# Performance work log

Hardware: AMD Instinct MI355X
Metric: run time of the kernel (lower is better)

The kernel has to match this reference:

```python
import jax, jax.numpy as jnp
import numpy as np

N_INPUT, N_HIDDEN, N_OUTPUT = 64, 512, 24

def setup_inputs() -> dict:
    key = jax.random.key(0)
    ks = jax.random.split(key, 7)
    s_ih = 1.0 / np.sqrt(N_HIDDEN)
    x = jax.random.normal(ks[0], (256, 512, N_INPUT), dtype=jnp.float32)
    W_ih = jax.random.uniform(ks[1], (N_HIDDEN, N_INPUT), minval=-s_ih, maxval=s_ih, dtype=jnp.float32)
    W_hh = jax.random.uniform(ks[2], (N_HIDDEN, N_HIDDEN), minval=-s_ih, maxval=s_ih, dtype=jnp.float32)
    b_ih = jax.random.uniform(ks[3], (N_HIDDEN,), minval=-s_ih, maxval=s_ih, dtype=jnp.float32)
    b_hh = jax.random.uniform(ks[4], (N_HIDDEN,), minval=-s_ih, maxval=s_ih, dtype=jnp.float32)
    W_ho = jax.random.uniform(ks[5], (N_OUTPUT, N_HIDDEN), minval=-s_ih, maxval=s_ih, dtype=jnp.float32)
    b_ho = jax.random.uniform(ks[6], (N_OUTPUT,), minval=-s_ih, maxval=s_ih, dtype=jnp.float32)
    return {"x": x, "W_ih": W_ih, "W_hh": W_hh, "b_ih": b_ih, "b_hh": b_hh, "W_ho": W_ho, "b_ho": b_ho}

def reference(x, W_ih, W_hh, b_ih, b_hh, W_ho, b_ho):
    B = x.shape[0]
    # Precompute input projections for all timesteps in one big GEMM: [B,T,H]
    xp = jnp.einsum('bti,hi->bth', x, W_ih) + b_ih + b_hh
    h0 = jnp.zeros((B, W_hh.shape[0]), dtype=x.dtype)

    def step(h, xp_t):
        h = jnp.tanh(xp_t + h @ W_hh.T)
        out = jnp.tanh(h @ W_ho.T + b_ho)
        return h, out

    _, outs = jax.lax.scan(step, h0, jnp.swapaxes(xp, 0, 1))  # outs: [T,B,O]
    return jnp.swapaxes(outs, 0, 1)  # [B,T,O]
```

## Files before the change

### kernel.cpp

```cpp
#include <hip/hip_runtime.h>
#include <cstdint>
#include <cstddef>


#define TSTEPS 512
#define HDIM   512
#define NIN    64
#define NOUT   24
#define BB     16
#define HPAD   520
#define XPAD   72
#define NREG   49
#define NLDS   (64 - NREG)
#define NREG_B 50
#define NLDS_B (64 - NREG_B)

typedef _Float16 h16;
typedef __attribute__((ext_vector_type(8))) _Float16 h16x8;
typedef __attribute__((ext_vector_type(4))) _Float16 h16x4;
typedef __attribute__((ext_vector_type(2))) _Float16 h16x2;
typedef __attribute__((ext_vector_type(4))) float    f32x4;
typedef __attribute__((ext_vector_type(2))) float    f32x2;

__device__ __forceinline__ float fast_tanh(float z) {
  float e = __builtin_amdgcn_exp2f(z * 2.8853900817779268f);
  return 1.0f - 2.0f * __builtin_amdgcn_rcpf(e + 1.0f);
}

__device__ __forceinline__ h16x8 cvt8(const float* __restrict__ p) {
  f32x4 f0 = *(const f32x4*)p;
  f32x4 f1 = *(const f32x4*)(p + 4);
  h16x8 a;
  #pragma unroll
  for (int j = 0; j < 4; ++j) { a[j] = (h16)f0[j]; a[4 + j] = (h16)f1[j]; }
  return a;
}

__global__ __launch_bounds__(512)
void xp_gemm(const float* __restrict__ x, const float* __restrict__ Wih,
             const float* __restrict__ bih, const float* __restrict__ bhh,
             h16* __restrict__ xp)
{
  const int tid  = threadIdx.x;
  const int wave = tid >> 6;
  const int lane = tid & 63;
  const int lr   = lane & 15;
  const int lk   = lane >> 4;
  const int blk  = blockIdx.x & 15;
  const int tc   = blockIdx.x >> 4;
  const int c0   = wave * 64;

  h16x8 A[4][2];
  #pragma unroll
  for (int m = 0; m < 4; ++m)
    #pragma unroll
    for (int s = 0; s < 2; ++s)
      A[m][s] = cvt8(Wih + (size_t)(c0 + 16 * m + lr) * NIN + 32 * s + 8 * lk);

  f32x4 bias[4];
  #pragma unroll
  for (int m = 0; m < 4; ++m) {
    const int c = c0 + 16 * m + 4 * lk;
    f32x4 bi = *(const f32x4*)&bih[c];
    f32x4 bh = *(const f32x4*)&bhh[c];
    bias[m] = bi + bh;
  }

  const float* xrow = x + (size_t)(16 * blk + lr) * (TSTEPS * NIN);

  for (int j = 0; j < 32; ++j) {
    const int t = tc * 32 + j;
    f32x4 acc[4];
    #pragma unroll
    for (int m = 0; m < 4; ++m) acc[m] = bias[m];
    #pragma unroll
    for (int s = 0; s < 2; ++s) {
      h16x8 bx = cvt8(xrow + (size_t)t * NIN + 32 * s + 8 * lk);
      #pragma unroll
      for (int m = 0; m < 4; ++m)
        acc[m] = __builtin_amdgcn_mfma_f32_16x16x32_f16(A[m][s], bx, acc[m], 0, 0, 0);
    }
    h16x8 c0v, c1v;
    #pragma unroll
    for (int i = 0; i < 4; ++i) {
      c0v[i]     = (h16)acc[0][i];
      c0v[4 + i] = (h16)acc[1][i];
      c1v[i]     = (h16)acc[2][i];
      c1v[4 + i] = (h16)acc[3][i];
    }
    h16* p = xp + ((((size_t)t * 16 + blk) * 8 + wave) * 64 + lane) * 16;
    *(h16x8*)p       = c0v;
    *(h16x8*)(p + 8) = c1v;
  }
}

__global__ __launch_bounds__(512, 2)
void rnn_core(const float* __restrict__ Whh, const h16* __restrict__ xp,
              h16* __restrict__ hall)
{
  __shared__ h16 hbuf[2][BB * HPAD];
  __shared__ h16 aslice[NLDS * 8 * 512];

  const int tid  = threadIdx.x;
  const int wave = tid >> 6;
  const int lane = tid & 63;
  const int lr   = lane & 15;
  const int lk   = lane >> 4;
  const int blk  = blockIdx.x;
  const int b0   = blk * BB;
  const int wc0  = wave * 64;

  h16x8 areg[NREG];
  #pragma unroll
  for (int s = 0; s < 16; ++s) {
    #pragma unroll
    for (int m = 0; m < 4; ++m) {
      h16x8 a = cvt8(Whh + (size_t)(wc0 + 16 * m + lr) * HDIM + 32 * s + 8 * lk);
      const int id = s * 4 + m;
      if (id < NREG) areg[id] = a;
      else *(h16x8*)&aslice[(size_t)((id - NREG) * 8 + wave) * 512 + lane * 8] = a;
    }
  }

  for (int idx = tid; idx < BB * HPAD; idx += 512) hbuf[0][idx] = (h16)0.f;
  __syncthreads();

  h16x8 xr0, xr1;
  {
    const h16* p = xp + (((size_t)blk * 8 + wave) * 64 + lane) * 16;
    xr0 = *(const h16x8*)p;
    xr1 = *(const h16x8*)(p + 8);
  }

  for (int t = 0; t < TSTEPS; ++t) {
    const h16* hb = hbuf[t & 1];
    h16*       hn = hbuf[(t + 1) & 1];

    f32x4 acc[4];
    #pragma unroll
    for (int i = 0; i < 4; ++i) {
      acc[0][i] = (float)xr0[i];
      acc[1][i] = (float)xr0[4 + i];
      acc[2][i] = (float)xr1[i];
      acc[3][i] = (float)xr1[4 + i];
    }

    {
      const int tn = (t + 1 < TSTEPS) ? (t + 1) : t;
      const h16* p = xp + ((((size_t)tn * 16 + blk) * 8 + wave) * 64 + lane) * 16;
      xr0 = *(const h16x8*)p;
      xr1 = *(const h16x8*)(p + 8);
    }

    #pragma unroll
    for (int s = 0; s < 16; ++s) {
      h16x8 bh = *(const h16x8*)&hb[lr * HPAD + 32 * s + 8 * lk];
      #pragma unroll
      for (int m = 0; m < 4; ++m) {
        const int id = s * 4 + m;
        h16x8 a = (id < NREG)
            ? areg[id]
            : *(const h16x8*)&aslice[(size_t)((id - NREG) * 8 + wave) * 512 + lane * 8];
        acc[m] = __builtin_amdgcn_mfma_f32_16x16x32_f16(a, bh, acc[m], 0, 0, 0);
      }
    }

    h16* hrow = hall + ((size_t)t * 256 + b0 + lr) * HDIM + wc0 + lk * 4;
    #pragma unroll
    for (int m = 0; m < 4; ++m) {
      h16x4 hv;
      #pragma unroll
      for (int i = 0; i < 4; ++i) hv[i] = (h16)fast_tanh(acc[m][i]);
      *(h16x4*)&hn[lr * HPAD + wc0 + 16 * m + 4 * lk] = hv;
      *(h16x4*)(hrow + 16 * m) = hv;
    }

    __syncthreads();
  }
}

__global__ __launch_bounds__(512)
void out_all(const h16* __restrict__ hall, const float* __restrict__ Who,
             const float* __restrict__ bho, float* __restrict__ out)
{
  __shared__ h16 wholds[NOUT * HPAD];

  const int tid  = threadIdx.x;
  const int wave = tid >> 6;
  const int lane = tid & 63;
  const int lr   = lane & 15;
  const int lk   = lane >> 4;

  for (int idx = tid; idx < NOUT * HDIM; idx += 512) {
    int r = idx >> 9, k = idx & 511;
    wholds[r * HPAD + k] = (h16)Who[idx];
  }

  f32x4 o0, o1;
  { o0 = *(const f32x4*)&bho[lk * 4]; }
  { int ob = 16 + lk * 4;
    if (ob < NOUT) o1 = *(const f32x4*)&bho[ob];
    else { o1[0] = 0.f; o1[1] = 0.f; o1[2] = 0.f; o1[3] = 0.f; } }
  __syncthreads();

  const int rt = blockIdx.x * 8 + wave;
  const int t  = rt >> 4;
  const int b  = (rt & 15) * 16 + lr;
  const int row1 = (16 + lr < NOUT) ? (16 + lr) : (8 + lr);

  const h16* hrow = hall + ((size_t)t * 256 + b) * HDIM + lk * 8;

  #pragma unroll
  for (int s = 0; s < 16; ++s) {
    h16x8 bh = *(const h16x8*)(hrow + 32 * s);
    h16x8 a0 = *(const h16x8*)&wholds[lr * HPAD + s * 32 + lk * 8];
    h16x8 a1 = *(const h16x8*)&wholds[row1 * HPAD + s * 32 + lk * 8];
    o0 = __builtin_amdgcn_mfma_f32_16x16x32_f16(a0, bh, o0, 0, 0, 0);
    o1 = __builtin_amdgcn_mfma_f32_16x16x32_f16(a1, bh, o1, 0, 0, 0);
  }

  float* op = out + ((size_t)b * TSTEPS + t) * NOUT;
  f32x4 v0;
  #pragma unroll
  for (int i = 0; i < 4; ++i) v0[i] = fast_tanh(o0[i]);
  *(f32x4*)(op + lk * 4) = v0;
  if (lk < 2) {
    f32x4 v1;
    #pragma unroll
    for (int i = 0; i < 4; ++i) v1[i] = fast_tanh(o1[i]);
    *(f32x4*)(op + 16 + lk * 4) = v1;
  }
}

__device__ __forceinline__ void out_proj(
    int t, const h16* __restrict__ hb, const h16* __restrict__ who,
    f32x4 bho0, f32x4 bho1, float* __restrict__ out, int b0, int lr, int lk)
{
  f32x4 o0 = bho0, o1 = bho1;
  const int row1 = (16 + lr < NOUT) ? (16 + lr) : (8 + lr);
  #pragma unroll
  for (int s = 0; s < 16; ++s) {
    h16x8 bh = *(const h16x8*)&hb[lr * HPAD + s * 32 + lk * 8];
    h16x8 a0 = *(const h16x8*)&who[lr * HPAD + s * 32 + lk * 8];
    h16x8 a1 = *(const h16x8*)&who[row1 * HPAD + s * 32 + lk * 8];
    o0 = __builtin_amdgcn_mfma_f32_16x16x32_f16(a0, bh, o0, 0, 0, 0);
    o1 = __builtin_amdgcn_mfma_f32_16x16x32_f16(a1, bh, o1, 0, 0, 0);
  }
  float* op = out + ((size_t)(b0 + lr) * TSTEPS + t) * NOUT;
  f32x4 v0;
  #pragma unroll
  for (int i = 0; i < 4; ++i) v0[i] = fast_tanh(o0[i]);
  *(f32x4*)(op + lk * 4) = v0;
  if (lk < 2) {
    f32x4 v1;
    #pragma unroll
    for (int i = 0; i < 4; ++i) v1[i] = fast_tanh(o1[i]);
    *(f32x4*)(op + 16 + lk * 4) = v1;
  }
}

__global__ __launch_bounds__(512, 2)
void rnn_fast2(const float* __restrict__ Whh, const float* __restrict__ Who,
               const float* __restrict__ bho, const h16* __restrict__ xp,
               float* __restrict__ out)
{
  __shared__ h16 hls[BB * HPAD];
  __shared__ h16 wholds[NOUT * HPAD];
  __shared__ h16 aslice[NLDS_B * 8 * 512];

  const int tid  = threadIdx.x;
  const int wave = tid >> 6;
  const int lane = tid & 63;
  const int lr   = lane & 15;
  const int lk   = lane >> 4;
  const int blk  = blockIdx.x;
  const int b0   = blk * BB;
  const int wc0  = wave * 64;

  h16x8 areg[NREG_B];
  #pragma unroll
  for (int s = 0; s < 16; ++s) {
    #pragma unroll
    for (int m = 0; m < 4; ++m) {
      h16x8 a = cvt8(Whh + (size_t)(wc0 + 16 * m + lr) * HDIM + 32 * s + 8 * lk);
      const int id = s * 4 + m;
      if (id < NREG_B) areg[id] = a;
      else *(h16x8*)&aslice[(size_t)((id - NREG_B) * 8 + wave) * 512 + lane * 8] = a;
    }
  }

  f32x4 bho0, bho1;
  { bho0 = *(const f32x4*)&bho[lk * 4]; }
  { int ob = 16 + lk * 4;
    if (ob < NOUT) bho1 = *(const f32x4*)&bho[ob];
    else { bho1[0] = 0.f; bho1[1] = 0.f; bho1[2] = 0.f; bho1[3] = 0.f; } }

  for (int idx = tid; idx < NOUT * HDIM; idx += 512) {
    int r = idx >> 9, k = idx & 511;
    wholds[r * HPAD + k] = (h16)Who[idx];
  }
  for (int idx = tid; idx < BB * HPAD; idx += 512) hls[idx] = (h16)0.f;
  __syncthreads();

  h16x8 xr0, xr1;
  {
    const h16* p = xp + (((size_t)blk * 8 + wave) * 64 + lane) * 16;
    xr0 = *(const h16x8*)p;
    xr1 = *(const h16x8*)(p + 8);
  }

  for (int t = 0; t < TSTEPS; ++t) {
    if (t > 0 && wave == ((t - 1) & 7))
      out_proj(t - 1, hls, wholds, bho0, bho1, out, b0, lr, lk);

    f32x4 acc[4];
    #pragma unroll
    for (int i = 0; i < 4; ++i) {
      acc[0][i] = (float)xr0[i];
      acc[1][i] = (float)xr0[4 + i];
      acc[2][i] = (float)xr1[i];
      acc[3][i] = (float)xr1[4 + i];
    }
    {
      const int tn = (t + 1 < TSTEPS) ? (t + 1) : t;
      const h16* p = xp + ((((size_t)tn * 16 + blk) * 8 + wave) * 64 + lane) * 16;
      xr0 = *(const h16x8*)p;
      xr1 = *(const h16x8*)(p + 8);
    }
    #pragma unroll
    for (int s = 0; s < 16; ++s) {
      h16x8 bh = *(const h16x8*)&hls[lr * HPAD + 32 * s + 8 * lk];
      #pragma unroll
      for (int m = 0; m < 4; ++m) {
        const int id = s * 4 + m;
        h16x8 a = (id < NREG_B)
            ? areg[id]
            : *(const h16x8*)&aslice[(size_t)((id - NREG_B) * 8 + wave) * 512 + lane * 8];
        acc[m] = __builtin_amdgcn_mfma_f32_16x16x32_f16(a, bh, acc[m], 0, 0, 0);
      }
    }
    __syncthreads();
    #pragma unroll
    for (int m = 0; m < 4; ++m) {
      h16x4 hv;
      #pragma unroll
      for (int i = 0; i < 4; ++i) hv[i] = (h16)fast_tanh(acc[m][i]);
      *(h16x4*)&hls[lr * HPAD + wc0 + 16 * m + 4 * lk] = hv;
    }
    __syncthreads();
  }

  if (wave == ((TSTEPS - 1) & 7))
    out_proj(TSTEPS - 1, hls, wholds, bho0, bho1, out, b0, lr, lk);
}

__global__ __launch_bounds__(512, 2)
void rnn_fused(const float* __restrict__ x,
               const float* __restrict__ Wih,
               const float* __restrict__ Whh,
               const float* __restrict__ bih,
               const float* __restrict__ bhh,
               const float* __restrict__ Who,
               const float* __restrict__ bho,
               float* __restrict__ out)
{
  __shared__ h16 hbuf[2][BB * HPAD];
  __shared__ h16 xbuf[2][BB * XPAD];
  __shared__ h16 wholds[NOUT * HPAD];

  const int tid  = threadIdx.x;
  const int wave = tid >> 6;
  const int lane = tid & 63;
  const int lr   = lane & 15;
  const int lk   = lane >> 4;
  const int b0   = blockIdx.x * BB;
  const int wc0  = wave * 64;

  h16x8 a_rec[4][16];
  #pragma unroll
  for (int m = 0; m < 4; ++m) {
    const int row = wc0 + m * 16 + lr;
    #pragma unroll
    for (int s = 0; s < 16; ++s)
      a_rec[m][s] = cvt8(Whh + (size_t)row * HDIM + s * 32 + lk * 8);
  }
  h16x8 a_ih[4][2];
  #pragma unroll
  for (int m = 0; m < 4; ++m) {
    const int row = wc0 + m * 16 + lr;
    #pragma unroll
    for (int s = 0; s < 2; ++s)
      a_ih[m][s] = cvt8(Wih + (size_t)row * NIN + s * 32 + lk * 8);
  }
  f32x4 biasv[4];
  #pragma unroll
  for (int m = 0; m < 4; ++m) {
    const int c = wc0 + m * 16 + lk * 4;
    f32x4 bi = *(const f32x4*)&bih[c];
    f32x4 bh2 = *(const f32x4*)&bhh[c];
    biasv[m] = bi + bh2;
  }
  f32x4 bho0, bho1;
  { bho0 = *(const f32x4*)&bho[lk * 4]; }
  { int ob = 16 + lk * 4;
    if (ob < NOUT) bho1 = *(const f32x4*)&bho[ob];
    else { bho1[0] = 0.f; bho1[1] = 0.f; bho1[2] = 0.f; bho1[3] = 0.f; } }

  for (int idx = tid; idx < NOUT * HDIM; idx += 512) {
    int r = idx >> 9, k = idx & 511;
    wholds[r * HPAD + k] = (h16)Who[idx];
  }
  for (int idx = tid; idx < BB * HPAD; idx += 512) hbuf[0][idx] = (h16)0.f;
  {
    int r = tid >> 5, c2 = (tid & 31) * 2;
    f32x2 v = *(const f32x2*)(x + ((size_t)(b0 + r) * TSTEPS + 0) * NIN + c2);
    h16x2 pk = { (h16)v.x, (h16)v.y };
    *(h16x2*)&xbuf[0][r * XPAD + c2] = pk;
  }
  __syncthreads();

  for (int t = 0; t < TSTEPS; ++t) {
    const h16* hb = hbuf[t & 1];
    h16*       hn = hbuf[(t + 1) & 1];
    const h16* xb = xbuf[t & 1];
    h16*       xn = xbuf[(t + 1) & 1];

    if (t > 0 && wave == ((t - 1) & 7))
      out_proj(t - 1, hb, wholds, bho0, bho1, out, b0, lr, lk);

    const int tl = (t + 1 < TSTEPS) ? (t + 1) : (TSTEPS - 1);
    const int xr = tid >> 5, xc = (tid & 31) * 2;
    f32x2 xv = *(const f32x2*)(x + ((size_t)(b0 + xr) * TSTEPS + tl) * NIN + xc);

    f32x4 acc[4];
    #pragma unroll
    for (int m = 0; m < 4; ++m) acc[m] = biasv[m];
    #pragma unroll
    for (int s = 0; s < 2; ++s) {
      h16x8 bx = *(const h16x8*)&xb[lr * XPAD + s * 32 + lk * 8];
      #pragma unroll
      for (int m = 0; m < 4; ++m)
        acc[m] = __builtin_amdgcn_mfma_f32_16x16x32_f16(a_ih[m][s], bx, acc[m], 0, 0, 0);
    }
    #pragma unroll
    for (int s = 0; s < 16; ++s) {
      h16x8 bh = *(const h16x8*)&hb[lr * HPAD + s * 32 + lk * 8];
      #pragma unroll
      for (int m = 0; m < 4; ++m)
        acc[m] = __builtin_amdgcn_mfma_f32_16x16x32_f16(a_rec[m][s], bh, acc[m], 0, 0, 0);
    }
    #pragma unroll
    for (int m = 0; m < 4; ++m) {
      h16x4 hv;
      #pragma unroll
      for (int i = 0; i < 4; ++i) hv[i] = (h16)fast_tanh(acc[m][i]);
      *(h16x4*)&hn[lr * HPAD + wc0 + m * 16 + lk * 4] = hv;
    }
    {
      h16x2 pk = { (h16)xv.x, (h16)xv.y };
      *(h16x2*)&xn[xr * XPAD + xc] = pk;
    }
    __syncthreads();
  }

  if (wave == ((TSTEPS - 1) & 7))
    out_proj(TSTEPS - 1, hbuf[TSTEPS & 1], wholds, bho0, bho1, out, b0, lr, lk);
}

extern "C" void kernel_launch(void* const* d_in, const int* in_sizes, int n_in,
                              void* d_out, int out_size, void* d_ws, size_t ws_size,
                              hipStream_t stream) {
  (void)in_sizes; (void)n_in; (void)out_size;
  const float* x   = (const float*)d_in[0];
  const float* Wih = (const float*)d_in[1];
  const float* Whh = (const float*)d_in[2];
  const float* bih = (const float*)d_in[3];
  const float* bhh = (const float*)d_in[4];
  const float* Who = (const float*)d_in[5];
  const float* bho = (const float*)d_in[6];
  float* out = (float*)d_out;

  const size_t XP_BYTES   = (size_t)TSTEPS * 256 * HDIM * sizeof(h16);
  const size_t HALL_BYTES = (size_t)TSTEPS * 256 * HDIM * sizeof(h16);

  if (ws_size >= XP_BYTES + HALL_BYTES) {
    h16* xp   = (h16*)d_ws;
    h16* hall = (h16*)((char*)d_ws + XP_BYTES);
    xp_gemm<<<dim3(256), dim3(512), 0, stream>>>(x, Wih, bih, bhh, xp);
    rnn_core<<<dim3(256 / BB), dim3(512), 0, stream>>>(Whh, xp, hall);
    out_all<<<dim3(1024), dim3(512), 0, stream>>>(hall, Who, bho, out);
  } else if (ws_size >= XP_BYTES) {
    h16* xp = (h16*)d_ws;
    xp_gemm<<<dim3(256), dim3(512), 0, stream>>>(x, Wih, bih, bhh, xp);
    rnn_fast2<<<dim3(256 / BB), dim3(512), 0, stream>>>(Whh, Who, bho, xp, out);
  } else {
    rnn_fused<<<dim3(256 / BB), dim3(512), 0, stream>>>(x, Wih, Whh, bih, bhh, Who, bho, out);
  }
}
```

Measured before the change: 1.090 ms.

## Split recurrent GEMM K-dimension across block pairs with global-memory partial-sum exchange

Adds rnn_core2, which splits each batch group's recurrent matmul over two workgroups, each holding half of the K dimension of W_hh entirely in registers and so dropping the LDS-resident weight slice. Each step, the non-finishing waves write fp32 partial sums to a global exchange buffer and signal an atomic counter; the finishing waves spin-wait, add the partner's partials, apply tanh and write h. This doubles the number of CUs working on the recurrence (32 blocks instead of 16) at the cost of a cross-CU handshake through L2 every timestep. The counter is zeroed inside xp_gemm, and the rnn_fast2 fallback path is removed.

```diff
diff --git a/kernel.cpp b/kernel.cpp
--- a/kernel.cpp
+++ b/kernel.cpp
@@ -10,10 +10,10 @@
 #define BB     16
 #define HPAD   520
 #define XPAD   72
+#define KHALF  256
+#define HPAD2  264
 #define NREG   49
 #define NLDS   (64 - NREG)
-#define NREG_B 50
-#define NLDS_B (64 - NREG_B)
 
 typedef _Float16 h16;
 typedef __attribute__((ext_vector_type(8))) _Float16 h16x8;
@@ -39,7 +39,7 @@
 __global__ __launch_bounds__(512)
 void xp_gemm(const float* __restrict__ x, const float* __restrict__ Wih,
              const float* __restrict__ bih, const float* __restrict__ bhh,
-             h16* __restrict__ xp)
+             h16* __restrict__ xp, unsigned* __restrict__ cnt)
 {
   const int tid  = threadIdx.x;
   const int wave = tid >> 6;
@@ -50,6 +50,8 @@
   const int tc   = blockIdx.x >> 4;
   const int c0   = wave * 64;
 
+  if (cnt && blockIdx.x == 0 && tid < 64) cnt[tid] = 0u;
+
   h16x8 A[4][2];
   #pragma unroll
   for (int m = 0; m < 4; ++m)
@@ -91,6 +93,155 @@
     h16* p = xp + ((((size_t)t * 16 + blk) * 8 + wave) * 64 + lane) * 16;
     *(h16x8*)p       = c0v;
     *(h16x8*)(p + 8) = c1v;
+  }
+}
+
+__global__ __launch_bounds__(512, 2)
+void rnn_core2(const float* __restrict__ Whh, const h16* __restrict__ xp,
+               h16* __restrict__ hall, float* __restrict__ ex,
+               unsigned* __restrict__ cnt)
+{
+  __shared__ h16 hl[2][16 * HPAD2];
+
+  const int tid  = threadIdx.x;
+  const int wave = tid >> 6;
+  const int lane = tid & 63;
+  const int lr   = lane & 15;
+  const int lk   = lane >> 4;
+  const int kb   = blockIdx.x >> 4;
+  const int g    = blockIdx.x & 15;
+  const int wq   = wave & 3;
+  const bool fin = ((wave >> 2) == kb);
+  const int b0   = g * 16;
+
+  h16x8 areg[8][4];
+  #pragma unroll
+  for (int s = 0; s < 8; ++s)
+    #pragma unroll
+    for (int m = 0; m < 4; ++m)
+      areg[s][m] = cvt8(Whh + (size_t)(64 * wave + 16 * m + lr) * HDIM
+                        + KHALF * kb + 32 * s + 8 * lk);
+
+  for (int idx = tid; idx < 16 * HPAD2; idx += 512) hl[0][idx] = (h16)0.f;
+  __syncthreads();
+
+  h16x8 xr0, xr1;
+  if (fin) {
+    const h16* p = xp + (((size_t)g * 8 + wave) * 64 + lane) * 16;
+    xr0 = *(const h16x8*)p;
+    xr1 = *(const h16x8*)(p + 8);
+  }
+
+  unsigned* mycnt   = &cnt[g * 2 + kb];
+  unsigned* partcnt = &cnt[g * 2 + (1 - kb)];
+
+  for (int t = 0; t < TSTEPS; ++t) {
+    f32x4 acc[4];
+    if (fin) {
+      #pragma unroll
+      for (int i = 0; i < 4; ++i) {
+        acc[0][i] = (float)xr0[i];
+        acc[1][i] = (float)xr0[4 + i];
+        acc[2][i] = (float)xr1[i];
+        acc[3][i] = (float)xr1[4 + i];
+      }
+      const int tn = (t + 1 < TSTEPS) ? (t + 1) : t;
+      const h16* p = xp + ((((size_t)tn * 16 + g) * 8 + wave) * 64 + lane) * 16;
+      xr0 = *(const h16x8*)p;
+      xr1 = *(const h16x8*)(p + 8);
+    } else {
+      #pragma unroll
+      for (int m = 0; m < 4; ++m) { acc[m][0]=0.f; acc[m][1]=0.f; acc[m][2]=0.f; acc[m][3]=0.f; }
+    }
+
+    const h16* hb = hl[t & 1];
+    #pragma unroll
+    for (int s = 0; s < 8; ++s) {
+      h16x8 bh = *(const h16x8*)&hb[lr * HPAD2 + 32 * s + 8 * lk];
+      #pragma unroll
+      for (int m = 0; m < 4; ++m)
+        acc[m] = __builtin_amdgcn_mfma_f32_16x16x32_f16(areg[s][m], bh, acc[m], 0, 0, 0);
+    }
+
+    if (!fin) {
+      float* exw = ex + ((size_t)((g * 2 + kb) * 2 + (t & 1)) << 12);
+      #pragma unroll
+      for (int m = 0; m < 4; ++m)
+        *(f32x4*)&exw[((wq * 16 + m * 4 + lk) << 6) + lr * 4] = acc[m];
+      if (lane == 0)
+        __hip_atomic_fetch_add(mycnt, 1u, __ATOMIC_RELEASE, __HIP_MEMORY_SCOPE_AGENT);
+    } else {
+      const unsigned tgt = 4u * (unsigned)(t + 1);
+      while (__hip_atomic_load(partcnt, __ATOMIC_ACQUIRE, __HIP_MEMORY_SCOPE_AGENT) < tgt)
+        __builtin_amdgcn_s_sleep(1);
+      const float* exr = ex + ((size_t)((g * 2 + (1 - kb)) * 2 + (t & 1)) << 12);
+      h16* hn   = hl[(t + 1) & 1];
+      h16* hrow = hall + ((size_t)t * 256 + b0 + lr) * HDIM + KHALF * kb + 64 * wq + 4 * lk;
+      #pragma unroll
+      for (int m = 0; m < 4; ++m) {
+        f32x4 pp = *(const f32x4*)&exr[((wq * 16 + m * 4 + lk) << 6) + lr * 4];
+        h16x4 hv;
+        #pragma unroll
+        for (int i = 0; i < 4; ++i) hv[i] = (h16)fast_tanh(acc[m][i] + pp[i]);
+        *(h16x4*)&hn[lr * HPAD2 + 64 * wq + 16 * m + 4 * lk] = hv;
+        *(h16x4*)(hrow + 16 * m) = hv;
+      }
+    }
+
+    __syncthreads();
+  }
+}
+
+__global__ __launch_bounds__(512)
+void out_all(const h16* __restrict__ hall, const float* __restrict__ Who,
+             const float* __restrict__ bho, float* __restrict__ out)
+{
+  __shared__ h16 wholds[NOUT * HPAD];
+
+  const int tid  = threadIdx.x;
+  const int wave = tid >> 6;
+  const int lane = tid & 63;
+  const int lr   = lane & 15;
+  const int lk   = lane >> 4;
+
+  for (int idx = tid; idx < NOUT * HDIM; idx += 512) {
+    int r = idx >> 9, k = idx & 511;
+    wholds[r * HPAD + k] = (h16)Who[idx];
+  }
+
+  f32x4 o0, o1;
+  { o0 = *(const f32x4*)&bho[lk * 4]; }
+  { int ob = 16 + lk * 4;
+    if (ob < NOUT) o1 = *(const f32x4*)&bho[ob];
+    else { o1[0] = 0.f; o1[1] = 0.f; o1[2] = 0.f; o1[3] = 0.f; } }
+  __syncthreads();
+
+  const int rt = blockIdx.x * 8 + wave;
+  const int t  = rt >> 4;
+  const int b  = (rt & 15) * 16 + lr;
+  const int row1 = (16 + lr < NOUT) ? (16 + lr) : (8 + lr);
+
+  const h16* hrow = hall + ((size_t)t * 256 + b) * HDIM + lk * 8;
+
+  #pragma unroll
+  for (int s = 0; s < 16; ++s) {
+    h16x8 bh = *(const h16x8*)(hrow + 32 * s);
+    h16x8 a0 = *(const h16x8*)&wholds[lr * HPAD + s * 32 + lk * 8];
+    h16x8 a1 = *(const h16x8*)&wholds[row1 * HPAD + s * 32 + lk * 8];
+    o0 = __builtin_amdgcn_mfma_f32_16x16x32_f16(a0, bh, o0, 0, 0, 0);
+    o1 = __builtin_amdgcn_mfma_f32_16x16x32_f16(a1, bh, o1, 0, 0, 0);
+  }
+
+  float* op = out + ((size_t)b * TSTEPS + t) * NOUT;
+  f32x4 v0;
+  #pragma unroll
+  for (int i = 0; i < 4; ++i) v0[i] = fast_tanh(o0[i]);
+  *(f32x4*)(op + lk * 4) = v0;
+  if (lk < 2) {
+    f32x4 v1;
+    #pragma unroll
+    for (int i = 0; i < 4; ++i) v1[i] = fast_tanh(o1[i]);
+    *(f32x4*)(op + 16 + lk * 4) = v1;
   }
 }
 
@@ -144,7 +295,6 @@
       acc[2][i] = (float)xr1[i];
       acc[3][i] = (float)xr1[4 + i];
     }
-
     {
       const int tn = (t + 1 < TSTEPS) ? (t + 1) : t;
       const h16* p = xp + ((((size_t)tn * 16 + blk) * 8 + wave) * 64 + lane) * 16;
@@ -179,59 +329,6 @@
   }
 }
 
-__global__ __launch_bounds__(512)
-void out_all(const h16* __restrict__ hall, const float* __restrict__ Who,
-             const float* __restrict__ bho, float* __restrict__ out)
-{
-  __shared__ h16 wholds[NOUT * HPAD];
-
-  const int tid  = threadIdx.x;
-  const int wave = tid >> 6;
-  const int lane = tid & 63;
-  const int lr   = lane & 15;
-  const int lk   = lane >> 4;
-
-  for (int idx = tid; idx < NOUT * HDIM; idx += 512) {
-    int r = idx >> 9, k = idx & 511;
-    wholds[r * HPAD + k] = (h16)Who[idx];
-  }
-
-  f32x4 o0, o1;
-  { o0 = *(const f32x4*)&bho[lk * 4]; }
-  { int ob = 16 + lk * 4;
-    if (ob < NOUT) o1 = *(const f32x4*)&bho[ob];
-    else { o1[0] = 0.f; o1[1] = 0.f; o1[2] = 0.f; o1[3] = 0.f; } }
-  __syncthreads();
-
-  const int rt = blockIdx.x * 8 + wave;
-  const int t  = rt >> 4;
-  const int b  = (rt & 15) * 16 + lr;
-  const int row1 = (16 + lr < NOUT) ? (16 + lr) : (8 + lr);
-
-  const h16* hrow = hall + ((size_t)t * 256 + b) * HDIM + lk * 8;
-
-  #pragma unroll
-  for (int s = 0; s < 16; ++s) {
-    h16x8 bh = *(const h16x8*)(hrow + 32 * s);
-    h16x8 a0 = *(const h16x8*)&wholds[lr * HPAD + s * 32 + lk * 8];
-    h16x8 a1 = *(const h16x8*)&wholds[row1 * HPAD + s * 32 + lk * 8];
-    o0 = __builtin_amdgcn_mfma_f32_16x16x32_f16(a0, bh, o0, 0, 0, 0);
-    o1 = __builtin_amdgcn_mfma_f32_16x16x32_f16(a1, bh, o1, 0, 0, 0);
-  }
-
-  float* op = out + ((size_t)b * TSTEPS + t) * NOUT;
-  f32x4 v0;
-  #pragma unroll
-  for (int i = 0; i < 4; ++i) v0[i] = fast_tanh(o0[i]);
-  *(f32x4*)(op + lk * 4) = v0;
-  if (lk < 2) {
-    f32x4 v1;
-    #pragma unroll
-    for (int i = 0; i < 4; ++i) v1[i] = fast_tanh(o1[i]);
-    *(f32x4*)(op + 16 + lk * 4) = v1;
-  }
-}
-
 __device__ __forceinline__ void out_proj(
     int t, const h16* __restrict__ hb, const h16* __restrict__ who,
     f32x4 bho0, f32x4 bho1, float* __restrict__ out, int b0, int lr, int lk)
@@ -257,101 +354,6 @@
     for (int i = 0; i < 4; ++i) v1[i] = fast_tanh(o1[i]);
     *(f32x4*)(op + 16 + lk * 4) = v1;
   }
-}
-
-__global__ __launch_bounds__(512, 2)
-void rnn_fast2(const float* __restrict__ Whh, const float* __restrict__ Who,
-               const float* __restrict__ bho, const h16* __restrict__ xp,
-               float* __restrict__ out)
-{
-  __shared__ h16 hls[BB * HPAD];
-  __shared__ h16 wholds[NOUT * HPAD];
-  __shared__ h16 aslice[NLDS_B * 8 * 512];
-
-  const int tid  = threadIdx.x;
-  const int wave = tid >> 6;
-  const int lane = tid & 63;
-  const int lr   = lane & 15;
-  const int lk   = lane >> 4;
-  const int blk  = blockIdx.x;
-  const int b0   = blk * BB;
-  const int wc0  = wave * 64;
-
-  h16x8 areg[NREG_B];
-  #pragma unroll
-  for (int s = 0; s < 16; ++s) {
-    #pragma unroll
-    for (int m = 0; m < 4; ++m) {
-      h16x8 a = cvt8(Whh + (size_t)(wc0 + 16 * m + lr) * HDIM + 32 * s + 8 * lk);
-      const int id = s * 4 + m;
-      if (id < NREG_B) areg[id] = a;
-      else *(h16x8*)&aslice[(size_t)((id - NREG_B) * 8 + wave) * 512 + lane * 8] = a;
-    }
-  }
-
-  f32x4 bho0, bho1;
-  { bho0 = *(const f32x4*)&bho[lk * 4]; }
-  { int ob = 16 + lk * 4;
-    if (ob < NOUT) bho1 = *(const f32x4*)&bho[ob];
-    else { bho1[0] = 0.f; bho1[1] = 0.f; bho1[2] = 0.f; bho1[3] = 0.f; } }
-
-  for (int idx = tid; idx < NOUT * HDIM; idx += 512) {
-    int r = idx >> 9, k = idx & 511;
-    wholds[r * HPAD + k] = (h16)Who[idx];
-  }
-  for (int idx = tid; idx < BB * HPAD; idx += 512) hls[idx] = (h16)0.f;
-  __syncthreads();
-
-  h16x8 xr0, xr1;
-  {
-    const h16* p = xp + (((size_t)blk * 8 + wave) * 64 + lane) * 16;
-    xr0 = *(const h16x8*)p;
-    xr1 = *(const h16x8*)(p + 8);
-  }
-
-  for (int t = 0; t < TSTEPS; ++t) {
-    if (t > 0 && wave == ((t - 1) & 7))
-      out_proj(t - 1, hls, wholds, bho0, bho1, out, b0, lr, lk);
-
-    f32x4 acc[4];
-    #pragma unroll
-    for (int i = 0; i < 4; ++i) {
-      acc[0][i] = (float)xr0[i];
-      acc[1][i] = (float)xr0[4 + i];
-      acc[2][i] = (float)xr1[i];
-      acc[3][i] = (float)xr1[4 + i];
-    }
-    {
-      const int tn = (t + 1 < TSTEPS) ? (t + 1) : t;
-      const h16* p = xp + ((((size_t)tn * 16 + blk) * 8 + wave) * 64 + lane) * 16;
-      xr0 = *(const h16x8*)p;
-      xr1 = *(const h16x8*)(p + 8);
-    }
-    #pragma unroll
-    for (int s = 0; s < 16; ++s) {
-      h16x8 bh = *(const h16x8*)&hls[lr * HPAD + 32 * s + 8 * lk];
-      #pragma unroll
-      for (int m = 0; m < 4; ++m) {
-        const int id = s * 4 + m;
-        h16x8 a = (id < NREG_B)
-            ? areg[id]
-            : *(const h16x8*)&aslice[(size_t)((id - NREG_B) * 8 + wave) * 512 + lane * 8];
-        acc[m] = __builtin_amdgcn_mfma_f32_16x16x32_f16(a, bh, acc[m], 0, 0, 0);
-      }
-    }
-    __syncthreads();
-    #pragma unroll
-    for (int m = 0; m < 4; ++m) {
-      h16x4 hv;
-      #pragma unroll
-      for (int i = 0; i < 4; ++i) hv[i] = (h16)fast_tanh(acc[m][i]);
-      *(h16x4*)&hls[lr * HPAD + wc0 + 16 * m + 4 * lk] = hv;
-    }
-    __syncthreads();
-  }
-
-  if (wave == ((TSTEPS - 1) & 7))
-    out_proj(TSTEPS - 1, hls, wholds, bho0, bho1, out, b0, lr, lk);
 }
 
 __global__ __launch_bounds__(512, 2)
@@ -444,7 +446,7 @@
     }
     #pragma unroll
     for (int s = 0; s < 16; ++s) {
-      h16x8 bh = *(const h16x8*)&hb[lr * HPAD + s * 32 + lk * 8];
+      h16x8 bh = *(const h16x8*)&hb[lr * HPAD + 32 * s + 8 * lk];
       #pragma unroll
       for (int m = 0; m < 4; ++m)
         acc[m] = __builtin_amdgcn_mfma_f32_16x16x32_f16(a_rec[m][s], bh, acc[m], 0, 0, 0);
@@ -454,7 +456,7 @@
       h16x4 hv;
       #pragma unroll
       for (int i = 0; i < 4; ++i) hv[i] = (h16)fast_tanh(acc[m][i]);
-      *(h16x4*)&hn[lr * HPAD + wc0 + m * 16 + lk * 4] = hv;
+      *(h16x4*)&hn[lr * HPAD + wc0 + 16 * m + 4 * lk] = hv;
     }
     {
       h16x2 pk = { (h16)xv.x, (h16)xv.y };
@@ -482,17 +484,23 @@
 
   const size_t XP_BYTES   = (size_t)TSTEPS * 256 * HDIM * sizeof(h16);
   const size_t HALL_BYTES = (size_t)TSTEPS * 256 * HDIM * sizeof(h16);
-
-  if (ws_size >= XP_BYTES + HALL_BYTES) {
+  const size_t EX_BYTES   = (size_t)64 * 4096 * sizeof(float);
+  const size_t CNT_BYTES  = 64 * sizeof(unsigned);
+
+  if (ws_size >= XP_BYTES + HALL_BYTES + EX_BYTES + CNT_BYTES) {
+    h16*      xp   = (h16*)d_ws;
+    h16*      hall = (h16*)((char*)d_ws + XP_BYTES);
+    float*    ex   = (float*)((char*)d_ws + XP_BYTES + HALL_BYTES);
+    unsigned* cnt  = (unsigned*)((char*)d_ws + XP_BYTES + HALL_BYTES + EX_BYTES);
+    xp_gemm<<<dim3(256), dim3(512), 0, stream>>>(x, Wih, bih, bhh, xp, cnt);
+    rnn_core2<<<dim3(32), dim3(512), 0, stream>>>(Whh, xp, hall, ex, cnt);
+    out_all<<<dim3(1024), dim3(512), 0, stream>>>(hall, Who, bho, out);
+  } else if (ws_size >= XP_BYTES + HALL_BYTES) {
     h16* xp   = (h16*)d_ws;
     h16* hall = (h16*)((char*)d_ws + XP_BYTES);
-    xp_gemm<<<dim3(256), dim3(512), 0, stream>>>(x, Wih, bih, bhh, xp);
+    xp_gemm<<<dim3(256), dim3(512), 0, stream>>>(x, Wih, bih, bhh, xp, nullptr);
     rnn_core<<<dim3(256 / BB), dim3(512), 0, stream>>>(Whh, xp, hall);
     out_all<<<dim3(1024), dim3(512), 0, stream>>>(hall, Who, bho, out);
-  } else if (ws_size >= XP_BYTES) {
-    h16* xp = (h16*)d_ws;
-    xp_gemm<<<dim3(256), dim3(512), 0, stream>>>(x, Wih, bih, bhh, xp);
-    rnn_fast2<<<dim3(256 / BB), dim3(512), 0, stream>>>(Whh, Who, bho, xp, out);
   } else {
     rnn_fused<<<dim3(256 / BB), dim3(512), 0, stream>>>(x, Wih, Whh, bih, bhh, Who, bho, out);
   }
```

After: 1.090 ms. Within noise of the previous version (+0.1%).

## Split W_hh fragments across registers, LDS and global scratch in output tail

Applied to the files above, without the earlier changes.

The recurrent kernel now keeps 50 W_hh fragments in registers, only 3 in LDS, and streams the remaining 11 from a pre-converted fp16 copy. The xp_gemm kernel writes that copy into the tail of the output buffer, which out_all overwrites later. This shrinks LDS use and LDS read traffic per step, and the per-step barrier becomes an explicit s_waitcnt lgkmcnt(0) plus s_barrier. The trade is extra global/L2 loads inside the serial time loop and reliance on scratch space in the output buffer. The rnn_fast2 path is removed.

```diff
diff --git a/kernel.cpp b/kernel.cpp
--- a/kernel.cpp
+++ b/kernel.cpp
@@ -10,10 +10,11 @@
 #define BB     16
 #define HPAD   520
 #define XPAD   72
-#define NREG   49
-#define NLDS   (64 - NREG)
-#define NREG_B 50
-#define NLDS_B (64 - NREG_B)
+#define NLDSL  3
+#define NREG   50
+#define NGLB   11
+#define WG_H16 (NGLB * 8 * 64 * 8)
+#define WG_F32 (WG_H16 / 2)
 
 typedef _Float16 h16;
 typedef __attribute__((ext_vector_type(8))) _Float16 h16x8;
@@ -39,7 +40,7 @@
 __global__ __launch_bounds__(512)
 void xp_gemm(const float* __restrict__ x, const float* __restrict__ Wih,
              const float* __restrict__ bih, const float* __restrict__ bhh,
-             h16* __restrict__ xp)
+             h16* __restrict__ xp, h16* wg, const float* __restrict__ Whh)
 {
   const int tid  = threadIdx.x;
   const int wave = tid >> 6;
@@ -50,6 +51,16 @@
   const int tc   = blockIdx.x >> 4;
   const int c0   = wave * 64;
 
+  if (wg && blockIdx.x == 0) {
+    #pragma unroll
+    for (int j = 0; j < NGLB; ++j) {
+      const int id = 53 + j;
+      const int s = id >> 2, m = id & 3;
+      h16x8 a = cvt8(Whh + (size_t)(c0 + 16 * m + lr) * HDIM + 32 * s + 8 * lk);
+      *(h16x8*)&wg[((size_t)(j * 8 + wave) * 64 + lane) * 8] = a;
+    }
+  }
+
   h16x8 A[4][2];
   #pragma unroll
   for (int m = 0; m < 4; ++m)
@@ -95,11 +106,11 @@
 }
 
 __global__ __launch_bounds__(512, 2)
-void rnn_core(const float* __restrict__ Whh, const h16* __restrict__ xp,
-              h16* __restrict__ hall)
+void rnn_core7(const float* __restrict__ Whh, const h16* __restrict__ xp,
+               h16* __restrict__ hall, const h16* wg)
 {
   __shared__ h16 hbuf[2][BB * HPAD];
-  __shared__ h16 aslice[NLDS * 8 * 512];
+  __shared__ h16 aslice[NLDSL * 8 * 512];
 
   const int tid  = threadIdx.x;
   const int wave = tid >> 6;
@@ -115,15 +126,20 @@
   for (int s = 0; s < 16; ++s) {
     #pragma unroll
     for (int m = 0; m < 4; ++m) {
+      const int id = s * 4 + m;
+      if (id >= NLDSL + NREG) continue;
       h16x8 a = cvt8(Whh + (size_t)(wc0 + 16 * m + lr) * HDIM + 32 * s + 8 * lk);
-      const int id = s * 4 + m;
-      if (id < NREG) areg[id] = a;
-      else *(h16x8*)&aslice[(size_t)((id - NREG) * 8 + wave) * 512 + lane * 8] = a;
+      if (id < NLDSL)
+        *(h16x8*)&aslice[(size_t)(id * 8 + wave) * 512 + lane * 8] = a;
+      else
+        areg[id - NLDSL] = a;
     }
   }
 
   for (int idx = tid; idx < BB * HPAD; idx += 512) hbuf[0][idx] = (h16)0.f;
   __syncthreads();
+
+  const h16* wgl = wg + (size_t)(wave * 64 + lane) * 8;
 
   h16x8 xr0, xr1;
   {
@@ -144,7 +160,6 @@
       acc[2][i] = (float)xr1[i];
       acc[3][i] = (float)xr1[4 + i];
     }
-
     {
       const int tn = (t + 1 < TSTEPS) ? (t + 1) : t;
       const h16* p = xp + ((((size_t)tn * 16 + blk) * 8 + wave) * 64 + lane) * 16;
@@ -158,9 +173,13 @@
       #pragma unroll
       for (int m = 0; m < 4; ++m) {
         const int id = s * 4 + m;
-        h16x8 a = (id < NREG)
-            ? areg[id]
-            : *(const h16x8*)&aslice[(size_t)((id - NREG) * 8 + wave) * 512 + lane * 8];
+        h16x8 a;
+        if (id >= NLDSL + NREG)
+          a = *(const h16x8*)&wgl[(size_t)(id - (NLDSL + NREG)) * 8 * 512];
+        else if (id < NLDSL)
+          a = *(const h16x8*)&aslice[(size_t)(id * 8 + wave) * 512 + lane * 8];
+        else
+          a = areg[id - NLDSL];
         acc[m] = __builtin_amdgcn_mfma_f32_16x16x32_f16(a, bh, acc[m], 0, 0, 0);
       }
     }
@@ -175,97 +194,17 @@
       *(h16x4*)(hrow + 16 * m) = hv;
     }
 
-    __syncthreads();
-  }
-}
-
-__global__ __launch_bounds__(512)
-void out_all(const h16* __restrict__ hall, const float* __restrict__ Who,
-             const float* __restrict__ bho, float* __restrict__ out)
+    asm volatile("s_waitcnt lgkmcnt(0)\n\ts_barrier" ::: "memory");
+  }
+}
+
+#define NREG_B 50
+#define NLDS_B (64 - NREG_B)
+__global__ __launch_bounds__(512, 2)
+void rnn_core6(const float* __restrict__ Whh, const h16* __restrict__ xp,
+               h16* __restrict__ hall)
 {
-  __shared__ h16 wholds[NOUT * HPAD];
-
-  const int tid  = threadIdx.x;
-  const int wave = tid >> 6;
-  const int lane = tid & 63;
-  const int lr   = lane & 15;
-  const int lk   = lane >> 4;
-
-  for (int idx = tid; idx < NOUT * HDIM; idx += 512) {
-    int r = idx >> 9, k = idx & 511;
-    wholds[r * HPAD + k] = (h16)Who[idx];
-  }
-
-  f32x4 o0, o1;
-  { o0 = *(const f32x4*)&bho[lk * 4]; }
-  { int ob = 16 + lk * 4;
-    if (ob < NOUT) o1 = *(const f32x4*)&bho[ob];
-    else { o1[0] = 0.f; o1[1] = 0.f; o1[2] = 0.f; o1[3] = 0.f; } }
-  __syncthreads();
-
-  const int rt = blockIdx.x * 8 + wave;
-  const int t  = rt >> 4;
-  const int b  = (rt & 15) * 16 + lr;
-  const int row1 = (16 + lr < NOUT) ? (16 + lr) : (8 + lr);
-
-  const h16* hrow = hall + ((size_t)t * 256 + b) * HDIM + lk * 8;
-
-  #pragma unroll
-  for (int s = 0; s < 16; ++s) {
-    h16x8 bh = *(const h16x8*)(hrow + 32 * s);
-    h16x8 a0 = *(const h16x8*)&wholds[lr * HPAD + s * 32 + lk * 8];
-    h16x8 a1 = *(const h16x8*)&wholds[row1 * HPAD + s * 32 + lk * 8];
-    o0 = __builtin_amdgcn_mfma_f32_16x16x32_f16(a0, bh, o0, 0, 0, 0);
-    o1 = __builtin_amdgcn_mfma_f32_16x16x32_f16(a1, bh, o1, 0, 0, 0);
-  }
-
-  float* op = out + ((size_t)b * TSTEPS + t) * NOUT;
-  f32x4 v0;
-  #pragma unroll
-  for (int i = 0; i < 4; ++i) v0[i] = fast_tanh(o0[i]);
-  *(f32x4*)(op + lk * 4) = v0;
-  if (lk < 2) {
-    f32x4 v1;
-    #pragma unroll
-    for (int i = 0; i < 4; ++i) v1[i] = fast_tanh(o1[i]);
-    *(f32x4*)(op + 16 + lk * 4) = v1;
-  }
-}
-
-__device__ __forceinline__ void out_proj(
-    int t, const h16* __restrict__ hb, const h16* __restrict__ who,
-    f32x4 bho0, f32x4 bho1, float* __restrict__ out, int b0, int lr, int lk)
-{
-  f32x4 o0 = bho0, o1 = bho1;
-  const int row1 = (16 + lr < NOUT) ? (16 + lr) : (8 + lr);
-  #pragma unroll
-  for (int s = 0; s < 16; ++s) {
-    h16x8 bh = *(const h16x8*)&hb[lr * HPAD + s * 32 + lk * 8];
-    h16x8 a0 = *(const h16x8*)&who[lr * HPAD + s * 32 + lk * 8];
-    h16x8 a1 = *(const h16x8*)&who[row1 * HPAD + s * 32 + lk * 8];
-    o0 = __builtin_amdgcn_mfma_f32_16x16x32_f16(a0, bh, o0, 0, 0, 0);
-    o1 = __builtin_amdgcn_mfma_f32_16x16x32_f16(a1, bh, o1, 0, 0, 0);
-  }
-  float* op = out + ((size_t)(b0 + lr) * TSTEPS + t) * NOUT;
-  f32x4 v0;
-  #pragma unroll
-  for (int i = 0; i < 4; ++i) v0[i] = fast_tanh(o0[i]);
-  *(f32x4*)(op + lk * 4) = v0;
-  if (lk < 2) {
-    f32x4 v1;
-    #pragma unroll
-    for (int i = 0; i < 4; ++i) v1[i] = fast_tanh(o1[i]);
-    *(f32x4*)(op + 16 + lk * 4) = v1;
-  }
-}
-
-__global__ __launch_bounds__(512, 2)
-void rnn_fast2(const float* __restrict__ Whh, const float* __restrict__ Who,
-               const float* __restrict__ bho, const h16* __restrict__ xp,
-               float* __restrict__ out)
-{
-  __shared__ h16 hls[BB * HPAD];
-  __shared__ h16 wholds[NOUT * HPAD];
+  __shared__ h16 hbuf[2][BB * HPAD];
   __shared__ h16 aslice[NLDS_B * 8 * 512];
 
   const int tid  = threadIdx.x;
@@ -289,17 +228,7 @@
     }
   }
 
-  f32x4 bho0, bho1;
-  { bho0 = *(const f32x4*)&bho[lk * 4]; }
-  { int ob = 16 + lk * 4;
-    if (ob < NOUT) bho1 = *(const f32x4*)&bho[ob];
-    else { bho1[0] = 0.f; bho1[1] = 0.f; bho1[2] = 0.f; bho1[3] = 0.f; } }
-
-  for (int idx = tid; idx < NOUT * HDIM; idx += 512) {
-    int r = idx >> 9, k = idx & 511;
-    wholds[r * HPAD + k] = (h16)Who[idx];
-  }
-  for (int idx = tid; idx < BB * HPAD; idx += 512) hls[idx] = (h16)0.f;
+  for (int idx = tid; idx < BB * HPAD; idx += 512) hbuf[0][idx] = (h16)0.f;
   __syncthreads();
 
   h16x8 xr0, xr1;
@@ -310,8 +239,8 @@
   }
 
   for (int t = 0; t < TSTEPS; ++t) {
-    if (t > 0 && wave == ((t - 1) & 7))
-      out_proj(t - 1, hls, wholds, bho0, bho1, out, b0, lr, lk);
+    const h16* hb = hbuf[t & 1];
+    h16*       hn = hbuf[(t + 1) & 1];
 
     f32x4 acc[4];
     #pragma unroll
@@ -327,9 +256,10 @@
       xr0 = *(const h16x8*)p;
       xr1 = *(const h16x8*)(p + 8);
     }
+
     #pragma unroll
     for (int s = 0; s < 16; ++s) {
-      h16x8 bh = *(const h16x8*)&hls[lr * HPAD + 32 * s + 8 * lk];
+      h16x8 bh = *(const h16x8*)&hb[lr * HPAD + 32 * s + 8 * lk];
       #pragma unroll
       for (int m = 0; m < 4; ++m) {
         const int id = s * 4 + m;
@@ -339,19 +269,99 @@
         acc[m] = __builtin_amdgcn_mfma_f32_16x16x32_f16(a, bh, acc[m], 0, 0, 0);
       }
     }
-    __syncthreads();
+
+    h16* hrow = hall + ((size_t)t * 256 + b0 + lr) * HDIM + wc0 + lk * 4;
     #pragma unroll
     for (int m = 0; m < 4; ++m) {
       h16x4 hv;
       #pragma unroll
       for (int i = 0; i < 4; ++i) hv[i] = (h16)fast_tanh(acc[m][i]);
-      *(h16x4*)&hls[lr * HPAD + wc0 + 16 * m + 4 * lk] = hv;
-    }
-    __syncthreads();
-  }
-
-  if (wave == ((TSTEPS - 1) & 7))
-    out_proj(TSTEPS - 1, hls, wholds, bho0, bho1, out, b0, lr, lk);
+      *(h16x4*)&hn[lr * HPAD + wc0 + 16 * m + 4 * lk] = hv;
+      *(h16x4*)(hrow + 16 * m) = hv;
+    }
+
+    asm volatile("s_waitcnt lgkmcnt(0)\n\ts_barrier" ::: "memory");
+  }
+}
+
+__global__ __launch_bounds__(512)
+void out_all(const h16* __restrict__ hall, const float* __restrict__ Who,
+             const float* __restrict__ bho, float* __restrict__ out)
+{
+  __shared__ h16 wholds[NOUT * HPAD];
+
+  const int tid  = threadIdx.x;
+  const int wave = tid >> 6;
+  const int lane = tid & 63;
+  const int lr   = lane & 15;
+  const int lk   = lane >> 4;
+
+  for (int idx = tid; idx < NOUT * HDIM; idx += 512) {
+    int r = idx >> 9, k = idx & 511;
+    wholds[r * HPAD + k] = (h16)Who[idx];
+  }
+
+  f32x4 o0, o1;
+  { o0 = *(const f32x4*)&bho[lk * 4]; }
+  { int ob = 16 + lk * 4;
+    if (ob < NOUT) o1 = *(const f32x4*)&bho[ob];
+    else { o1[0] = 0.f; o1[1] = 0.f; o1[2] = 0.f; o1[3] = 0.f; } }
+  __syncthreads();
+
+  const int rt = blockIdx.x * 8 + wave;
+  const int t  = rt >> 4;
+  const int b  = (rt & 15) * 16 + lr;
+  const int row1 = (16 + lr < NOUT) ? (16 + lr) : (8 + lr);
+
+  const h16* hrow = hall + ((size_t)t * 256 + b) * HDIM + lk * 8;
+
+  #pragma unroll
+  for (int s = 0; s < 16; ++s) {
+    h16x8 bh = *(const h16x8*)(hrow + 32 * s);
+    h16x8 a0 = *(const h16x8*)&wholds[lr * HPAD + s * 32 + lk * 8];
+    h16x8 a1 = *(const h16x8*)&wholds[row1 * HPAD + s * 32 + lk * 8];
+    o0 = __builtin_amdgcn_mfma_f32_16x16x32_f16(a0, bh, o0, 0, 0, 0);
+    o1 = __builtin_amdgcn_mfma_f32_16x16x32_f16(a1, bh, o1, 0, 0, 0);
+  }
+
+  float* op = out + ((size_t)b * TSTEPS + t) * NOUT;
+  f32x4 v0;
+  #pragma unroll
+  for (int i = 0; i < 4; ++i) v0[i] = fast_tanh(o0[i]);
+  *(f32x4*)(op + lk * 4) = v0;
+  if (lk < 2) {
+    f32x4 v1;
+    #pragma unroll
+    for (int i = 0; i < 4; ++i) v1[i] = fast_tanh(o1[i]);
+    *(f32x4*)(op + 16 + lk * 4) = v1;
+  }
+}
+
+__device__ __forceinline__ void out_proj(
+    int t, const h16* __restrict__ hb, const h16* __restrict__ who,
+    f32x4 bho0, f32x4 bho1, float* __restrict__ out, int b0, int lr, int lk)
+{
+  f32x4 o0 = bho0, o1 = bho1;
+  const int row1 = (16 + lr < NOUT) ? (16 + lr) : (8 + lr);
+  #pragma unroll
+  for (int s = 0; s < 16; ++s) {
+    h16x8 bh = *(const h16x8*)&hb[lr * HPAD + s * 32 + lk * 8];
+    h16x8 a0 = *(const h16x8*)&who[lr * HPAD + s * 32 + lk * 8];
+    h16x8 a1 = *(const h16x8*)&who[row1 * HPAD + s * 32 + lk * 8];
+    o0 = __builtin_amdgcn_mfma_f32_16x16x32_f16(a0, bh, o0, 0, 0, 0);
+    o1 = __builtin_amdgcn_mfma_f32_16x16x32_f16(a1, bh, o1, 0, 0, 0);
+  }
+  float* op = out + ((size_t)(b0 + lr) * TSTEPS + t) * NOUT;
+  f32x4 v0;
+  #pragma unroll
+  for (int i = 0; i < 4; ++i) v0[i] = fast_tanh(o0[i]);
+  *(f32x4*)(op + lk * 4) = v0;
+  if (lk < 2) {
+    f32x4 v1;
+    #pragma unroll
+    for (int i = 0; i < 4; ++i) v1[i] = fast_tanh(o1[i]);
+    *(f32x4*)(op + 16 + lk * 4) = v1;
+  }
 }
 
 __global__ __launch_bounds__(512, 2)
@@ -444,7 +454,7 @@
     }
     #pragma unroll
     for (int s = 0; s < 16; ++s) {
-      h16x8 bh = *(const h16x8*)&hb[lr * HPAD + s * 32 + lk * 8];
+      h16x8 bh = *(const h16x8*)&hb[lr * HPAD + 32 * s + 8 * lk];
       #pragma unroll
       for (int m = 0; m < 4; ++m)
         acc[m] = __builtin_amdgcn_mfma_f32_16x16x32_f16(a_rec[m][s], bh, acc[m], 0, 0, 0);
@@ -454,7 +464,7 @@
       h16x4 hv;
       #pragma unroll
       for (int i = 0; i < 4; ++i) hv[i] = (h16)fast_tanh(acc[m][i]);
-      *(h16x4*)&hn[lr * HPAD + wc0 + m * 16 + lk * 4] = hv;
+      *(h16x4*)&hn[lr * HPAD + wc0 + 16 * m + 4 * lk] = hv;
     }
     {
       h16x2 pk = { (h16)xv.x, (h16)xv.y };
@@ -470,7 +480,7 @@
 extern "C" void kernel_launch(void* const* d_in, const int* in_sizes, int n_in,
                               void* d_out, int out_size, void* d_ws, size_t ws_size,
                               hipStream_t stream) {
-  (void)in_sizes; (void)n_in; (void)out_size;
+  (void)in_sizes; (void)n_in;
   const float* x   = (const float*)d_in[0];
   const float* Wih = (const float*)d_in[1];
   const float* Whh = (const float*)d_in[2];
@@ -486,13 +496,16 @@
   if (ws_size >= XP_BYTES + HALL_BYTES) {
     h16* xp   = (h16*)d_ws;
     h16* hall = (h16*)((char*)d_ws + XP_BYTES);
-    xp_gemm<<<dim3(256), dim3(512), 0, stream>>>(x, Wih, bih, bhh, xp);
-    rnn_core<<<dim3(256 / BB), dim3(512), 0, stream>>>(Whh, xp, hall);
+    const bool wg_ok = (out_size >= 2 * WG_F32) && ((out_size & 3) == 0);
+    if (wg_ok) {
+      h16* wg = (h16*)(out + ((size_t)out_size - WG_F32));
+      xp_gemm<<<dim3(256), dim3(512), 0, stream>>>(x, Wih, bih, bhh, xp, wg, Whh);
+      rnn_core7<<<dim3(16), dim3(512), 0, stream>>>(Whh, xp, hall, wg);
+    } else {
+      xp_gemm<<<dim3(256), dim3(512), 0, stream>>>(x, Wih, bih, bhh, xp, nullptr, Whh);
+      rnn_core6<<<dim3(16), dim3(512), 0, stream>>>(Whh, xp, hall);
+    }
     out_all<<<dim3(1024), dim3(512), 0, stream>>>(hall, Who, bho, out);
-  } else if (ws_size >= XP_BYTES) {
-    h16* xp = (h16*)d_ws;
-    xp_gemm<<<dim3(256), dim3(512), 0, stream>>>(x, Wih, bih, bhh, xp);
-    rnn_fast2<<<dim3(256 / BB), dim3(512), 0, stream>>>(Whh, Who, bho, xp, out);
   } else {
     rnn_fused<<<dim3(256 / BB), dim3(512), 0, stream>>>(x, Wih, Whh, bih, bhh, Who, bho, out);
   }
```

Measured after the change: 1.774 ms. 62.8% more time.
